# Kernel optimization log

Measured on AMD Instinct MI355X. Metric: run time of the kernel, lower is better.

## Reference

```python
import jax, jax.numpy as jnp
import numpy as np

EMBD = 768
N_HEADS = 12
HEAD_SIZE = EMBD // N_HEADS  # 64


def setup_inputs() -> dict:
    key = jax.random.key(0)
    kx, kq, kk, kv = jax.random.split(key, 4)
    B, S = 4, 4096
    x = jax.random.normal(kx, (B, S, EMBD), dtype=jnp.float32)
    # nn.Linear(embd, head_size, bias=False): y = x @ W.T with W [head_size, embd].
    # We store the transposed weight [embd, head_size] and apply x @ Wq, same math.
    scale = 1.0 / np.sqrt(EMBD)
    Wq = jax.random.normal(kq, (EMBD, HEAD_SIZE), dtype=jnp.float32) * scale
    Wk = jax.random.normal(kk, (EMBD, HEAD_SIZE), dtype=jnp.float32) * scale
    Wv = jax.random.normal(kv, (EMBD, HEAD_SIZE), dtype=jnp.float32) * scale
    return {"x": x, "Wq": Wq, "Wk": Wk, "Wv": Wv}


def reference(x, Wq, Wk, Wv):
    # q, k, v: [B, S, head_size]
    q = jnp.einsum("bse,eh->bsh", x, Wq)
    k = jnp.einsum("bse,eh->bsh", x, Wk)
    v = jnp.einsum("bse,eh->bsh", x, Wv)
    scale = jnp.asarray(HEAD_SIZE, q.dtype) ** -0.5
    # scores: [B, S, S]
    scores = jnp.einsum("bqh,bkh->bqk", q, k) * scale
    S = x.shape[1]
    causal = jnp.tril(jnp.ones((S, S), dtype=bool))
    scores = jnp.where(causal, scores, jnp.asarray(-jnp.inf, scores.dtype))
    weights = jax.nn.softmax(scores, axis=-1)
    # attn_dropout = 0.0 -> identity
    out = jnp.einsum("bqk,bkh->bqh", weights, v)  # [B, S, head_size]
    return out
```

## Files before the change

### kernel.cpp

```cpp
#include <hip/hip_runtime.h>

#define EMBD 768
#define HS 64
#define S_LEN 4096
#define BK 64

typedef __attribute__((ext_vector_type(8))) short short8;
typedef __attribute__((ext_vector_type(4))) short short4_t;
typedef __attribute__((ext_vector_type(4))) float f32x4;
typedef unsigned short ushort_t;
typedef unsigned int uint_t;

static __device__ __forceinline__ ushort_t f2bf(float f) {
    union { float f; unsigned u; } x; x.f = f;
    unsigned r = x.u + 0x7fffu + ((x.u >> 16) & 1u);
    return (ushort_t)(r >> 16);
}

static __device__ __forceinline__ uint_t cvt_pk_bf16(float lo, float hi) {
    uint_t r;
    asm volatile("v_cvt_pk_bf16_f32 %0, %1, %2" : "=v"(r) : "v"(lo), "v"(hi));
    return r;
}

static __device__ __forceinline__ short8 pack_bf8(float4 a, float4 b) {
    union { short8 s; uint_t u[4]; } r;
    r.u[0] = cvt_pk_bf16(a.x, a.y); r.u[1] = cvt_pk_bf16(a.z, a.w);
    r.u[2] = cvt_pk_bf16(b.x, b.y); r.u[3] = cvt_pk_bf16(b.z, b.w);
    return r.s;
}

static __device__ __forceinline__ void gl_lds16(const void* g, void* l) {
    __builtin_amdgcn_global_load_lds(
        (const __attribute__((address_space(1))) unsigned int*)g,
        (__attribute__((address_space(3))) unsigned int*)l, 16, 0, 0);
}

__global__ __launch_bounds__(256) void wprep_kernel(
    const float* __restrict__ Wq, const float* __restrict__ Wk, const float* __restrict__ Wv,
    ushort_t* __restrict__ Wt)
{
    __shared__ float ws[64][65];
    const int blk  = blockIdx.x;
    const int widx = blk / 12, kblk = blk % 12;
    const float* W = (widx == 0) ? Wq : (widx == 1) ? Wk : Wv;
    const int k0 = kblk * 64;
    const int t  = threadIdx.x;
    const int r  = t >> 2, c0 = (t & 3) * 16;
#pragma unroll
    for (int i = 0; i < 4; ++i) {
        float4 v = *(const float4*)(W + (size_t)(k0 + r) * HS + c0 + i * 4);
        ws[c0 + i*4 + 0][r] = v.x; ws[c0 + i*4 + 1][r] = v.y;
        ws[c0 + i*4 + 2][r] = v.z; ws[c0 + i*4 + 3][r] = v.w;
    }
    __syncthreads();
    const int c = t >> 2, kc = (t & 3) * 16;
    ushort_t* dst = Wt + (size_t)(widx * 64 + c) * EMBD + k0 + kc;
#pragma unroll
    for (int i = 0; i < 4; ++i) {
        short4_t p = {(short)f2bf(ws[c][kc + i*4 + 0]), (short)f2bf(ws[c][kc + i*4 + 1]),
                      (short)f2bf(ws[c][kc + i*4 + 2]), (short)f2bf(ws[c][kc + i*4 + 3])};
        *(short4_t*)(dst + i * 4) = p;
    }
}

__global__ __launch_bounds__(512) void qkv_kernel(
    const float* __restrict__ x, const ushort_t* __restrict__ Wt,
    ushort_t* __restrict__ Qg, ushort_t* __restrict__ Kg, ushort_t* __restrict__ Vtg)
{
    __shared__ char xA[2][16384];
    __shared__ char Wl[2][24576];
    __shared__ float Vs[64][65];
    const int t    = threadIdx.x;
    const int w    = t >> 6;
    const int lane = t & 63;
    const int l15  = lane & 15;
    const int l4   = lane >> 4;
    const int mg   = w >> 2;
    const int cg   = w & 3;
    const int row0 = blockIdx.x * 64;

    const int arow_s0 = t >> 4,          ag0 = t & 15;
    const int arow_s1 = (512 + t) >> 4,  ag1 = t & 15;
    const float* asrc0 = x + (size_t)(row0 + arow_s0) * EMBD + ((ag0 ^ (arow_s0 & 15)) << 2);
    const float* asrc1 = x + (size_t)(row0 + arow_s1) * EMBD + ((ag1 ^ (arow_s1 & 15)) << 2);
    const int wc0 = t >> 3,           wg0 = t & 7;
    const int wc1 = (512 + t) >> 3,   wg1 = t & 7;
    const int wc2 = (1024 + t) >> 3,  wg2 = t & 7;
    const ushort_t* wsrc0 = Wt + (size_t)wc0 * EMBD + ((wg0 ^ (wc0 & 7)) << 3);
    const ushort_t* wsrc1 = Wt + (size_t)wc1 * EMBD + ((wg1 ^ (wc1 & 7)) << 3);
    const ushort_t* wsrc2 = Wt + (size_t)wc2 * EMBD + ((wg2 ^ (wc2 & 7)) << 3);

    auto stage = [&](int kt, int buf) {
        const int xo = kt * 64;
        gl_lds16(asrc0 + xo, xA[buf] + w * 1024);
        gl_lds16(asrc1 + xo, xA[buf] + 8192 + w * 1024);
        gl_lds16(wsrc0 + xo, Wl[buf] + w * 1024);
        gl_lds16(wsrc1 + xo, Wl[buf] + 8192 + w * 1024);
        gl_lds16(wsrc2 + xo, Wl[buf] + 16384 + w * 1024);
    };

    const int ar0 = mg * 32 + l15;
    const int ar1 = mg * 32 + 16 + l15;
    const int wcol0 = cg * 48 + l15;
    const int wcol1 = cg * 48 + 16 + l15;
    const int wcol2 = cg * 48 + 32 + l15;

    f32x4 acc[2][3];
#pragma unroll
    for (int i = 0; i < 2; ++i)
#pragma unroll
        for (int j = 0; j < 3; ++j) acc[i][j] = (f32x4){0.f, 0.f, 0.f, 0.f};

    stage(0, 0);
    __syncthreads();

#pragma unroll
    for (int kt = 0; kt < 12; ++kt) {
        const int cur = kt & 1;
        if (kt < 11) stage(kt + 1, cur ^ 1);
        const char* Ab = xA[cur];
        const char* Wb = Wl[cur];
#pragma unroll
        for (int ks = 0; ks < 2; ++ks) {
            const int gf = ks * 8 + l4 * 2;
            float4 a00 = *(const float4*)(Ab + ar0 * 256 + (((gf    ) ^ (ar0 & 15)) << 4));
            float4 a01 = *(const float4*)(Ab + ar0 * 256 + (((gf + 1) ^ (ar0 & 15)) << 4));
            float4 a10 = *(const float4*)(Ab + ar1 * 256 + (((gf    ) ^ (ar1 & 15)) << 4));
            float4 a11 = *(const float4*)(Ab + ar1 * 256 + (((gf + 1) ^ (ar1 & 15)) << 4));
            short8 af0 = pack_bf8(a00, a01);
            short8 af1 = pack_bf8(a10, a11);
            const int gw = ks * 4 + l4;
            short8 wf0 = *(const short8*)(Wb + wcol0 * 128 + ((gw ^ (wcol0 & 7)) << 4));
            short8 wf1 = *(const short8*)(Wb + wcol1 * 128 + ((gw ^ (wcol1 & 7)) << 4));
            short8 wf2 = *(const short8*)(Wb + wcol2 * 128 + ((gw ^ (wcol2 & 7)) << 4));
            acc[0][0] = __builtin_amdgcn_mfma_f32_16x16x32_bf16(af0, wf0, acc[0][0], 0, 0, 0);
            acc[0][1] = __builtin_amdgcn_mfma_f32_16x16x32_bf16(af0, wf1, acc[0][1], 0, 0, 0);
            acc[0][2] = __builtin_amdgcn_mfma_f32_16x16x32_bf16(af0, wf2, acc[0][2], 0, 0, 0);
            acc[1][0] = __builtin_amdgcn_mfma_f32_16x16x32_bf16(af1, wf0, acc[1][0], 0, 0, 0);
            acc[1][1] = __builtin_amdgcn_mfma_f32_16x16x32_bf16(af1, wf1, acc[1][1], 0, 0, 0);
            acc[1][2] = __builtin_amdgcn_mfma_f32_16x16x32_bf16(af1, wf2, acc[1][2], 0, 0, 0);
        }
        if (kt < 11) __syncthreads();
    }

#pragma unroll
    for (int rf = 0; rf < 2; ++rf) {
        const int lrow = mg * 32 + rf * 16 + l4 * 4;
        const size_t grow = (size_t)row0 + lrow;
#pragma unroll
        for (int ct = 0; ct < 3; ++ct) {
            const int cbase = cg * 48 + ct * 16;
            const int sel   = cbase >> 6;
            const int cloc  = (cbase & 63) + l15;
#pragma unroll
            for (int r = 0; r < 4; ++r) {
                const float v = acc[rf][ct][r];
                if (sel == 0)      Qg[(grow + r) * HS + cloc] = f2bf(v * 0.125f);
                else if (sel == 1) Kg[(grow + r) * HS + cloc] = f2bf(v);
                else               Vs[lrow + r][cloc] = v;
            }
        }
    }
    __syncthreads();
    {
        const int vcol = t >> 3, vr0 = (t & 7) * 8;
        const int bb = row0 >> 12, s0 = row0 & 4095;
        union { short8 s; uint_t u[4]; } vp;
#pragma unroll
        for (int i = 0; i < 4; ++i)
            vp.u[i] = cvt_pk_bf16(Vs[vr0 + i * 2][vcol], Vs[vr0 + i * 2 + 1][vcol]);
        *(short8*)(Vtg + ((size_t)bb * HS + vcol) * S_LEN + s0 + vr0) = vp.s;
    }
}

__global__ __launch_bounds__(256) void attn_kernel(
    const ushort_t* __restrict__ Qg, const ushort_t* __restrict__ Kg,
    const ushort_t* __restrict__ Vtg,
    float* __restrict__ pacc, float* __restrict__ pm, float* __restrict__ pl)
{
    __shared__ char smem[40960];
    const int t    = threadIdx.x;
    const int w    = t >> 6;
    const int lane = t & 63;
    const int l15  = lane & 15;
    const int l4   = lane >> 4;

    const int g     = blockIdx.x;
    const int b     = g >> 7;
    const int inner = g & 127;
    const int jp    = inner >> 2;
    const int v     = inner & 3;

    const ushort_t* Kb_ = Kg  + (size_t)b * S_LEN * HS;
    const ushort_t* Vb_ = Vtg + (size_t)b * HS * S_LEN;
    const ushort_t* Qb_ = Qg  + (size_t)b * S_LEN * HS;

    char* myP = smem + 32768 + w * 2048;
    const int psw = (l15 & 7) << 4;

    auto stage = [&](int k0, int db) {
#pragma unroll
        for (int i = 0; i < 2; ++i) {
            const int row = w * 16 + i * 8 + (lane >> 3);
            const int c   = lane & 7;
            gl_lds16(Kb_ + (size_t)(k0 + row) * HS + ((c ^ (row & 7)) * 8),
                     smem + db * 8192 + w * 2048 + i * 1024);
            gl_lds16(Vb_ + (size_t)row * S_LEN + k0 + ((c ^ (row & 7)) * 8),
                     smem + 16384 + db * 8192 + w * 2048 + i * 1024);
        }
    };

    auto run_phase = [&](int r, int pidx) {
        const int q0r = r * BK;
        const int nt  = r + 1;
        const int q   = q0r + w * 16 + l15;
        const ushort_t* qrow = Qb_ + (size_t)q * HS;
        short8 qf0 = *(const short8*)(qrow + l4 * 8);
        short8 qf1 = *(const short8*)(qrow + 32 + l4 * 8);
        f32x4 acc[4];
#pragma unroll
        for (int j = 0; j < 4; ++j) acc[j] = (f32x4){0.f,0.f,0.f,0.f};
        float mm = -3e38f, ls = 0.f;

        __syncthreads();
        if (v < nt) stage(v * BK, 0);
        int db = 0;
        for (int tt = v; tt < nt; tt += 4, db ^= 1) {
            __syncthreads();
            if (tt + 4 < nt) stage((tt + 4) * BK, db ^ 1);
            const char* Kt  = smem + db * 8192;
            const char* Vt2 = smem + 16384 + db * 8192;

            f32x4 sT[4];
#pragma unroll
            for (int st = 0; st < 4; ++st) {
                const int krow = st * 16 + l15;
                const char* krb = Kt + krow * 128;
                const int sw = krow & 7;
                short8 kc0 = *(const short8*)(krb + ((l4 ^ sw) << 4));
                short8 kc1 = *(const short8*)(krb + (((4 + l4) ^ sw) << 4));
                f32x4 z = (f32x4){0.f,0.f,0.f,0.f};
                z = __builtin_amdgcn_mfma_f32_16x16x32_bf16(kc0, qf0, z, 0, 0, 0);
                z = __builtin_amdgcn_mfma_f32_16x16x32_bf16(kc1, qf1, z, 0, 0, 0);
                sT[st] = z;
            }
            if (tt == r) {
#pragma unroll
                for (int st = 0; st < 4; ++st)
#pragma unroll
                    for (int rr = 0; rr < 4; ++rr)
                        if (tt * BK + st * 16 + l4 * 4 + rr > q) sT[st][rr] = -3e38f;
            }
            float a0 = fmaxf(fmaxf(sT[0][0], sT[0][1]), fmaxf(sT[0][2], sT[0][3]));
            float a1 = fmaxf(fmaxf(sT[1][0], sT[1][1]), fmaxf(sT[1][2], sT[1][3]));
            float a2 = fmaxf(fmaxf(sT[2][0], sT[2][1]), fmaxf(sT[2][2], sT[2][3]));
            float a3 = fmaxf(fmaxf(sT[3][0], sT[3][1]), fmaxf(sT[3][2], sT[3][3]));
            float mt = fmaxf(fmaxf(a0, a1), fmaxf(a2, a3));
            if (__any(mt > mm + 8.f)) {
                mt = fmaxf(mt, __shfl_xor(mt, 16));
                mt = fmaxf(mt, __shfl_xor(mt, 32));
                float mn = fmaxf(mm, mt);
                float corr = __expf(mm - mn);
                ls *= corr;
#pragma unroll
                for (int ds = 0; ds < 4; ++ds)
#pragma unroll
                    for (int rr = 0; rr < 4; ++rr) acc[ds][rr] *= corr;
                mm = mn;
            }
            char* pr = myP + l15 * 128;
            float la = 0.f;
#pragma unroll
            for (int st = 0; st < 4; ++st) {
                float p0 = __expf(sT[st][0] - mm);
                float p1 = __expf(sT[st][1] - mm);
                float p2 = __expf(sT[st][2] - mm);
                float p3 = __expf(sT[st][3] - mm);
                la += (p0 + p1) + (p2 + p3);
                uint2 pk; pk.x = cvt_pk_bf16(p0, p1); pk.y = cvt_pk_bf16(p2, p3);
                *(uint2*)(pr + ((st * 32 + l4 * 8) ^ psw)) = pk;
            }
            ls += la;
            short8 pb0 = *(const short8*)(pr + ((l4 * 16) ^ psw));
            short8 pb1 = *(const short8*)(pr + ((64 + l4 * 16) ^ psw));
#pragma unroll
            for (int ds = 0; ds < 4; ++ds) {
                const int vrow = ds * 16 + l15;
                const char* vrb = Vt2 + vrow * 128;
                const int sw2 = vrow & 7;
                short8 v0 = *(const short8*)(vrb + ((l4 ^ sw2) << 4));
                short8 v1 = *(const short8*)(vrb + (((4 + l4) ^ sw2) << 4));
                acc[ds] = __builtin_amdgcn_mfma_f32_16x16x32_bf16(v0, pb0, acc[ds], 0, 0, 0);
                acc[ds] = __builtin_amdgcn_mfma_f32_16x16x32_bf16(v1, pb1, acc[ds], 0, 0, 0);
            }
        }

        ls += __shfl_xor(ls, 16);
        ls += __shfl_xor(ls, 32);
        float* pa = pacc + ((size_t)pidx * 64 + w * 16 + l15) * 64 + l4 * 4;
#pragma unroll
        for (int ds = 0; ds < 4; ++ds) *(f32x4*)(pa + ds * 16) = acc[ds];
        if (l4 == 0) {
            pm[pidx * 64 + w * 16 + l15] = mm;
            pl[pidx * 64 + w * 16 + l15] = ls;
        }
    };

    run_phase(jp,      (b * 64 + jp) * 4 + v);
    run_phase(63 - jp, (b * 64 + 63 - jp) * 4 + v);
}

__global__ __launch_bounds__(256) void combine_kernel(
    const float* __restrict__ pacc, const float* __restrict__ pm, const float* __restrict__ pl,
    float* __restrict__ out)
{
    const int g   = blockIdx.x;
    const int t   = threadIdx.x;
    const int row = t >> 2;
    const int d0  = (t & 3) * 16;
    float mv[4], lv[4];
#pragma unroll
    for (int p = 0; p < 4; ++p) {
        mv[p] = pm[(g * 4 + p) * 64 + row];
        lv[p] = pl[(g * 4 + p) * 64 + row];
    }
    float ms = fmaxf(fmaxf(mv[0], mv[1]), fmaxf(mv[2], mv[3]));
    float e[4], ll = 0.f;
#pragma unroll
    for (int p = 0; p < 4; ++p) { e[p] = __expf(mv[p] - ms); ll += lv[p] * e[p]; }
    const float inv = 1.f / ll;
    float4* op = (float4*)&out[((size_t)g * 64 + row) * 64 + d0];
#pragma unroll
    for (int i = 0; i < 4; ++i) {
        float4 o = make_float4(0.f, 0.f, 0.f, 0.f);
#pragma unroll
        for (int p = 0; p < 4; ++p) {
            float4 a = *(const float4*)&pacc[((size_t)(g * 4 + p) * 64 + row) * 64 + d0 + i * 4];
            o.x += a.x * e[p]; o.y += a.y * e[p]; o.z += a.z * e[p]; o.w += a.w * e[p];
        }
        op[i] = make_float4(o.x * inv, o.y * inv, o.z * inv, o.w * inv);
    }
}

extern "C" void kernel_launch(void* const* d_in, const int* in_sizes, int n_in,
                              void* d_out, int out_size, void* d_ws, size_t ws_size,
                              hipStream_t stream) {
    const float* x  = (const float*)d_in[0];
    const float* Wq = (const float*)d_in[1];
    const float* Wk = (const float*)d_in[2];
    const float* Wv = (const float*)d_in[3];
    float* out = (float*)d_out;

    const int rows = in_sizes[0] / EMBD;
    const int B    = rows / S_LEN;

    ushort_t* Qb = (ushort_t*)d_ws;
    ushort_t* Kb = Qb + (size_t)rows * HS;
    ushort_t* Vt = Kb + (size_t)rows * HS;
    ushort_t* Wt = Vt + (size_t)rows * HS;
    float* pacc = (float*)(Wt + 192 * EMBD);
    float* pm   = pacc + (size_t)B * 64 * 4 * 64 * 64;
    float* pl   = pm + (size_t)B * 64 * 4 * 64;

    hipLaunchKernelGGL(wprep_kernel, dim3(36), dim3(256), 0, stream, Wq, Wk, Wv, Wt);
    hipLaunchKernelGGL(qkv_kernel, dim3(rows / 64), dim3(512), 0, stream,
                       x, Wt, Qb, Kb, Vt);
    hipLaunchKernelGGL(attn_kernel, dim3(B * 128), dim3(256), 0, stream,
                       Qb, Kb, Vt, pacc, pm, pl);
    hipLaunchKernelGGL(combine_kernel, dim3(B * 64), dim3(256), 0, stream,
                       pacc, pm, pl, out);
}
```

Measured before the change: 56.65 us.

## Shrink QKV projection tiles to 32 rows and store attention partials as bf16

The QKV projection kernel now handles 32 rows per block with a 32-wide K step instead of 64x64. This doubles the grid to 512 blocks and cuts LDS per block so more of the GPU stays occupied, at the cost of twice as many K iterations and barriers. Separately, the attention kernel writes its partial accumulators as bf16 rather than fp32, and the combine kernel reads and upconverts them. This halves the partial-buffer traffic between the two kernels but adds rounding error to the unnormalized partial outputs.

```diff
diff --git a/kernel.cpp b/kernel.cpp
--- a/kernel.cpp
+++ b/kernel.cpp
@@ -15,6 +15,10 @@
     union { float f; unsigned u; } x; x.f = f;
     unsigned r = x.u + 0x7fffu + ((x.u >> 16) & 1u);
     return (ushort_t)(r >> 16);
+}
+
+static __device__ __forceinline__ float bf2f(ushort_t u) {
+    union { float f; uint_t u; } x; x.u = ((uint_t)u) << 16; return x.f;
 }
 
 static __device__ __forceinline__ uint_t cvt_pk_bf16(float lo, float hi) {
@@ -68,9 +72,9 @@
     const float* __restrict__ x, const ushort_t* __restrict__ Wt,
     ushort_t* __restrict__ Qg, ushort_t* __restrict__ Kg, ushort_t* __restrict__ Vtg)
 {
-    __shared__ char xA[2][16384];
-    __shared__ char Wl[2][24576];
-    __shared__ float Vs[64][65];
+    __shared__ char xA[2][4096];
+    __shared__ char Wl[2][12288];
+    __shared__ float Vs[32][65];
     const int t    = threadIdx.x;
     const int w    = t >> 6;
     const int lane = t & 63;
@@ -78,106 +82,90 @@
     const int l4   = lane >> 4;
     const int mg   = w >> 2;
     const int cg   = w & 3;
-    const int row0 = blockIdx.x * 64;
-
-    const int arow_s0 = t >> 4,          ag0 = t & 15;
-    const int arow_s1 = (512 + t) >> 4,  ag1 = t & 15;
-    const float* asrc0 = x + (size_t)(row0 + arow_s0) * EMBD + ((ag0 ^ (arow_s0 & 15)) << 2);
-    const float* asrc1 = x + (size_t)(row0 + arow_s1) * EMBD + ((ag1 ^ (arow_s1 & 15)) << 2);
-    const int wc0 = t >> 3,           wg0 = t & 7;
-    const int wc1 = (512 + t) >> 3,   wg1 = t & 7;
-    const int wc2 = (1024 + t) >> 3,  wg2 = t & 7;
-    const ushort_t* wsrc0 = Wt + (size_t)wc0 * EMBD + ((wg0 ^ (wc0 & 7)) << 3);
-    const ushort_t* wsrc1 = Wt + (size_t)wc1 * EMBD + ((wg1 ^ (wc1 & 7)) << 3);
-    const ushort_t* wsrc2 = Wt + (size_t)wc2 * EMBD + ((wg2 ^ (wc2 & 7)) << 3);
+    const int row0 = blockIdx.x * 32;
+
+    const float* g1srcA = 0; const ushort_t* g1srcW = 0;
+    if (t < 256) {
+        const int row = t >> 3, gi = t & 7;
+        g1srcA = x + (size_t)(row0 + row) * EMBD + ((gi ^ (row & 7)) << 2);
+    } else {
+        const int c = (t - 256) >> 2, gi = t & 3;
+        const int sc = (c & 3) ^ ((c >> 2) & 3);
+        g1srcW = Wt + (size_t)c * EMBD + ((gi ^ sc) << 3);
+    }
+    const int c2 = 64 + (t >> 2), gi2 = t & 3;
+    const int sc2 = (c2 & 3) ^ ((c2 >> 2) & 3);
+    const ushort_t* g2srcW = Wt + (size_t)c2 * EMBD + ((gi2 ^ sc2) << 3);
 
     auto stage = [&](int kt, int buf) {
-        const int xo = kt * 64;
-        gl_lds16(asrc0 + xo, xA[buf] + w * 1024);
-        gl_lds16(asrc1 + xo, xA[buf] + 8192 + w * 1024);
-        gl_lds16(wsrc0 + xo, Wl[buf] + w * 1024);
-        gl_lds16(wsrc1 + xo, Wl[buf] + 8192 + w * 1024);
-        gl_lds16(wsrc2 + xo, Wl[buf] + 16384 + w * 1024);
+        const int xo = kt * 32;
+        if (t < 256) gl_lds16(g1srcA + xo, xA[buf] + (w & 3) * 1024);
+        else         gl_lds16(g1srcW + xo, Wl[buf] + (w - 4) * 1024);
+        gl_lds16(g2srcW + xo, Wl[buf] + 4096 + w * 1024);
     };
 
-    const int ar0 = mg * 32 + l15;
-    const int ar1 = mg * 32 + 16 + l15;
-    const int wcol0 = cg * 48 + l15;
-    const int wcol1 = cg * 48 + 16 + l15;
-    const int wcol2 = cg * 48 + 32 + l15;
-
-    f32x4 acc[2][3];
-#pragma unroll
-    for (int i = 0; i < 2; ++i)
-#pragma unroll
-        for (int j = 0; j < 3; ++j) acc[i][j] = (f32x4){0.f, 0.f, 0.f, 0.f};
+    const int ar = mg * 16 + l15;
+    const int wc0 = cg * 48 + l15;
+    const int wc1 = wc0 + 16, wc2 = wc0 + 32;
+    const int swc0 = l4 ^ (wc0 & 3) ^ ((wc0 >> 2) & 3);
+    const int swc1 = l4 ^ (wc1 & 3) ^ ((wc1 >> 2) & 3);
+    const int swc2 = l4 ^ (wc2 & 3) ^ ((wc2 >> 2) & 3);
+
+    f32x4 acc[3];
+#pragma unroll
+    for (int j = 0; j < 3; ++j) acc[j] = (f32x4){0.f, 0.f, 0.f, 0.f};
 
     stage(0, 0);
     __syncthreads();
 
 #pragma unroll
-    for (int kt = 0; kt < 12; ++kt) {
+    for (int kt = 0; kt < 24; ++kt) {
         const int cur = kt & 1;
-        if (kt < 11) stage(kt + 1, cur ^ 1);
+        if (kt < 23) stage(kt + 1, cur ^ 1);
         const char* Ab = xA[cur];
         const char* Wb = Wl[cur];
-#pragma unroll
-        for (int ks = 0; ks < 2; ++ks) {
-            const int gf = ks * 8 + l4 * 2;
-            float4 a00 = *(const float4*)(Ab + ar0 * 256 + (((gf    ) ^ (ar0 & 15)) << 4));
-            float4 a01 = *(const float4*)(Ab + ar0 * 256 + (((gf + 1) ^ (ar0 & 15)) << 4));
-            float4 a10 = *(const float4*)(Ab + ar1 * 256 + (((gf    ) ^ (ar1 & 15)) << 4));
-            float4 a11 = *(const float4*)(Ab + ar1 * 256 + (((gf + 1) ^ (ar1 & 15)) << 4));
-            short8 af0 = pack_bf8(a00, a01);
-            short8 af1 = pack_bf8(a10, a11);
-            const int gw = ks * 4 + l4;
-            short8 wf0 = *(const short8*)(Wb + wcol0 * 128 + ((gw ^ (wcol0 & 7)) << 4));
-            short8 wf1 = *(const short8*)(Wb + wcol1 * 128 + ((gw ^ (wcol1 & 7)) << 4));
-            short8 wf2 = *(const short8*)(Wb + wcol2 * 128 + ((gw ^ (wcol2 & 7)) << 4));
-            acc[0][0] = __builtin_amdgcn_mfma_f32_16x16x32_bf16(af0, wf0, acc[0][0], 0, 0, 0);
-            acc[0][1] = __builtin_amdgcn_mfma_f32_16x16x32_bf16(af0, wf1, acc[0][1], 0, 0, 0);
-            acc[0][2] = __builtin_amdgcn_mfma_f32_16x16x32_bf16(af0, wf2, acc[0][2], 0, 0, 0);
-            acc[1][0] = __builtin_amdgcn_mfma_f32_16x16x32_bf16(af1, wf0, acc[1][0], 0, 0, 0);
-            acc[1][1] = __builtin_amdgcn_mfma_f32_16x16x32_bf16(af1, wf1, acc[1][1], 0, 0, 0);
-            acc[1][2] = __builtin_amdgcn_mfma_f32_16x16x32_bf16(af1, wf2, acc[1][2], 0, 0, 0);
-        }
-        if (kt < 11) __syncthreads();
-    }
-
-#pragma unroll
-    for (int rf = 0; rf < 2; ++rf) {
-        const int lrow = mg * 32 + rf * 16 + l4 * 4;
-        const size_t grow = (size_t)row0 + lrow;
-#pragma unroll
-        for (int ct = 0; ct < 3; ++ct) {
-            const int cbase = cg * 48 + ct * 16;
-            const int sel   = cbase >> 6;
-            const int cloc  = (cbase & 63) + l15;
-#pragma unroll
-            for (int r = 0; r < 4; ++r) {
-                const float v = acc[rf][ct][r];
-                if (sel == 0)      Qg[(grow + r) * HS + cloc] = f2bf(v * 0.125f);
-                else if (sel == 1) Kg[(grow + r) * HS + cloc] = f2bf(v);
-                else               Vs[lrow + r][cloc] = v;
-            }
+        float4 a0 = *(const float4*)(Ab + ar * 128 + (((2 * l4)     ^ (ar & 7)) << 4));
+        float4 a1 = *(const float4*)(Ab + ar * 128 + (((2 * l4 + 1) ^ (ar & 7)) << 4));
+        short8 af = pack_bf8(a0, a1);
+        short8 wf0 = *(const short8*)(Wb + wc0 * 64 + (swc0 << 4));
+        short8 wf1 = *(const short8*)(Wb + wc1 * 64 + (swc1 << 4));
+        short8 wf2 = *(const short8*)(Wb + wc2 * 64 + (swc2 << 4));
+        acc[0] = __builtin_amdgcn_mfma_f32_16x16x32_bf16(af, wf0, acc[0], 0, 0, 0);
+        acc[1] = __builtin_amdgcn_mfma_f32_16x16x32_bf16(af, wf1, acc[1], 0, 0, 0);
+        acc[2] = __builtin_amdgcn_mfma_f32_16x16x32_bf16(af, wf2, acc[2], 0, 0, 0);
+        if (kt < 23) __syncthreads();
+    }
+
+    const int lrow = mg * 16 + l4 * 4;
+    const size_t grow = (size_t)row0 + lrow;
+#pragma unroll
+    for (int ct = 0; ct < 3; ++ct) {
+        const int cbase = cg * 48 + ct * 16;
+        const int sel   = cbase >> 6;
+        const int cloc  = (cbase & 63) + l15;
+#pragma unroll
+        for (int r = 0; r < 4; ++r) {
+            const float v = acc[ct][r];
+            if (sel == 0)      Qg[(grow + r) * HS + cloc] = f2bf(v * 0.125f);
+            else if (sel == 1) Kg[(grow + r) * HS + cloc] = f2bf(v);
+            else               Vs[lrow + r][cloc] = v;
         }
     }
     __syncthreads();
     {
-        const int vcol = t >> 3, vr0 = (t & 7) * 8;
+        const int vcol = t >> 3, vr0 = (t & 7) * 4;
         const int bb = row0 >> 12, s0 = row0 & 4095;
-        union { short8 s; uint_t u[4]; } vp;
-#pragma unroll
-        for (int i = 0; i < 4; ++i)
-            vp.u[i] = cvt_pk_bf16(Vs[vr0 + i * 2][vcol], Vs[vr0 + i * 2 + 1][vcol]);
-        *(short8*)(Vtg + ((size_t)bb * HS + vcol) * S_LEN + s0 + vr0) = vp.s;
+        union { short4_t s; uint_t u[2]; } vp;
+        vp.u[0] = cvt_pk_bf16(Vs[vr0][vcol],     Vs[vr0 + 1][vcol]);
+        vp.u[1] = cvt_pk_bf16(Vs[vr0 + 2][vcol], Vs[vr0 + 3][vcol]);
+        *(short4_t*)(Vtg + ((size_t)bb * HS + vcol) * S_LEN + s0 + vr0) = vp.s;
     }
 }
 
 __global__ __launch_bounds__(256) void attn_kernel(
     const ushort_t* __restrict__ Qg, const ushort_t* __restrict__ Kg,
     const ushort_t* __restrict__ Vtg,
-    float* __restrict__ pacc, float* __restrict__ pm, float* __restrict__ pl)
+    ushort_t* __restrict__ pacc, float* __restrict__ pm, float* __restrict__ pl)
 {
     __shared__ char smem[40960];
     const int t    = threadIdx.x;
@@ -298,9 +286,14 @@
 
         ls += __shfl_xor(ls, 16);
         ls += __shfl_xor(ls, 32);
-        float* pa = pacc + ((size_t)pidx * 64 + w * 16 + l15) * 64 + l4 * 4;
-#pragma unroll
-        for (int ds = 0; ds < 4; ++ds) *(f32x4*)(pa + ds * 16) = acc[ds];
+        ushort_t* pa = pacc + ((size_t)pidx * 64 + w * 16 + l15) * 64 + l4 * 4;
+#pragma unroll
+        for (int ds = 0; ds < 4; ++ds) {
+            uint2 pk;
+            pk.x = cvt_pk_bf16(acc[ds][0], acc[ds][1]);
+            pk.y = cvt_pk_bf16(acc[ds][2], acc[ds][3]);
+            *(uint2*)(pa + ds * 16) = pk;
+        }
         if (l4 == 0) {
             pm[pidx * 64 + w * 16 + l15] = mm;
             pl[pidx * 64 + w * 16 + l15] = ls;
@@ -312,7 +305,7 @@
 }
 
 __global__ __launch_bounds__(256) void combine_kernel(
-    const float* __restrict__ pacc, const float* __restrict__ pm, const float* __restrict__ pl,
+    const ushort_t* __restrict__ pacc, const float* __restrict__ pm, const float* __restrict__ pl,
     float* __restrict__ out)
 {
     const int g   = blockIdx.x;
@@ -330,17 +323,24 @@
 #pragma unroll
     for (int p = 0; p < 4; ++p) { e[p] = __expf(mv[p] - ms); ll += lv[p] * e[p]; }
     const float inv = 1.f / ll;
+    float o[16];
+#pragma unroll
+    for (int i = 0; i < 16; ++i) o[i] = 0.f;
+#pragma unroll
+    for (int p = 0; p < 4; ++p) {
+        const ushort_t* src = pacc + ((size_t)(g * 4 + p) * 64 + row) * 64 + d0;
+        short8 s0 = *(const short8*)(src);
+        short8 s1 = *(const short8*)(src + 8);
+#pragma unroll
+        for (int i = 0; i < 8; ++i) {
+            o[i]     += bf2f((ushort_t)s0[i]) * e[p];
+            o[8 + i] += bf2f((ushort_t)s1[i]) * e[p];
+        }
+    }
     float4* op = (float4*)&out[((size_t)g * 64 + row) * 64 + d0];
 #pragma unroll
-    for (int i = 0; i < 4; ++i) {
-        float4 o = make_float4(0.f, 0.f, 0.f, 0.f);
-#pragma unroll
-        for (int p = 0; p < 4; ++p) {
-            float4 a = *(const float4*)&pacc[((size_t)(g * 4 + p) * 64 + row) * 64 + d0 + i * 4];
-            o.x += a.x * e[p]; o.y += a.y * e[p]; o.z += a.z * e[p]; o.w += a.w * e[p];
-        }
-        op[i] = make_float4(o.x * inv, o.y * inv, o.z * inv, o.w * inv);
-    }
+    for (int i = 0; i < 4; ++i)
+        op[i] = make_float4(o[i*4] * inv, o[i*4+1] * inv, o[i*4+2] * inv, o[i*4+3] * inv);
 }
 
 extern "C" void kernel_launch(void* const* d_in, const int* in_sizes, int n_in,
@@ -359,12 +359,12 @@
     ushort_t* Kb = Qb + (size_t)rows * HS;
     ushort_t* Vt = Kb + (size_t)rows * HS;
     ushort_t* Wt = Vt + (size_t)rows * HS;
-    float* pacc = (float*)(Wt + 192 * EMBD);
-    float* pm   = pacc + (size_t)B * 64 * 4 * 64 * 64;
-    float* pl   = pm + (size_t)B * 64 * 4 * 64;
+    ushort_t* pacc = Wt + 192 * EMBD;
+    float* pm = (float*)(pacc + (size_t)B * 64 * 4 * 64 * 64);
+    float* pl = pm + (size_t)B * 64 * 4 * 64;
 
     hipLaunchKernelGGL(wprep_kernel, dim3(36), dim3(256), 0, stream, Wq, Wk, Wv, Wt);
-    hipLaunchKernelGGL(qkv_kernel, dim3(rows / 64), dim3(512), 0, stream,
+    hipLaunchKernelGGL(qkv_kernel, dim3(rows / 32), dim3(512), 0, stream,
                        x, Wt, Qb, Kb, Vt);
     hipLaunchKernelGGL(attn_kernel, dim3(B * 128), dim3(256), 0, stream,
                        Qb, Kb, Vt, pacc, pm, pl);
```

Result: faster. 54.88 us (-3.1%).
